# Performance work log

Hardware: AMD Instinct MI355X
Metric: run time of the kernel (lower is better)

The kernel has to match this reference:

```python
import jax, jax.numpy as jnp
import numpy as np

C, C_H, N_HEAD = 8, 1, 8


def setup_inputs() -> dict:
    key = jax.random.key(0)
    ks = jax.random.split(key, 8)
    B, S, I, c = 1, 4096, 1024, C
    hd = C_H * N_HEAD
    m = jax.random.normal(ks[0], (B, S, I, c), dtype=jnp.float32)
    mask = jnp.ones((B, S, I), dtype=jnp.float32)
    return {
        "m": m,
        "mask": mask,
        "ln_w": jnp.ones((c,), jnp.float32),
        "ln_b": jnp.zeros((c,), jnp.float32),
        "wq": jax.random.normal(ks[1], (hd, c), jnp.float32) * 0.1,
        "wk": jax.random.normal(ks[2], (C_H, c), jnp.float32) * 0.1,
        "wv": jax.random.normal(ks[3], (C_H, c), jnp.float32) * 0.1,
        "wg": jax.random.normal(ks[4], (hd, c), jnp.float32) * 0.1,
        "bg": jnp.zeros((hd,), jnp.float32),
        "wo": jax.random.normal(ks[5], (c, hd), jnp.float32) * 0.1,
        "bo": jnp.zeros((c,), jnp.float32),
    }


def _layer_norm(x, w, b, eps=1e-5):
    mu = jnp.mean(x, axis=-1, keepdims=True)
    var = jnp.mean(jnp.square(x - mu), axis=-1, keepdims=True)
    return (x - mu) * jax.lax.rsqrt(var + eps) * w + b


def reference(m, mask, ln_w, ln_b, wq, wk, wv, wg, bg, wo, bo):
    h, c_h = N_HEAD, C_H
    # transpose so attention runs over the sequence (column) axis s
    mt = jnp.swapaxes(m, -2, -3)        # (B, i, s, c)
    mk = jnp.swapaxes(mask, -1, -2)     # (B, i, s)
    mn = _layer_norm(mt, ln_w, ln_b)    # (B, i, s, c)
    # masked mean-pooled query over s
    q = jnp.sum(mn * mk[..., None], axis=-2) / (jnp.sum(mk, axis=-1)[..., None] + 1e-5)  # (B,i,c)
    q = (q @ wq.T) * (c_h ** -0.5)                      # (B, i, h*c_h)
    q = q.reshape(*q.shape[:-1], h, c_h)                # (B, i, h, c_h)
    k = mn @ wk.T                                       # (B, i, s, c_h)
    v = mn @ wv.T                                       # (B, i, s, c_h)
    g = jax.nn.sigmoid(mn @ wg.T + bg)                  # (B, i, s, h*c_h)
    g = g.reshape(*g.shape[:-1], h, c_h)                # (B, i, s, h, c_h)
    bias = (1e9 * (mk - 1.0))[..., None, :]             # (B, i, 1, s)
    a = jnp.einsum('bihd,bisd->bihs', q, k) + bias      # (B, i, h, s)
    a = jax.nn.softmax(a, axis=-1)
    o = jnp.einsum('bihs,bisd->bihd', a, v)             # (B, i, h, c_h)
    o = o[..., None, :, :] * g                          # (B, i, s, h, c_h)
    o = o.reshape(*o.shape[:-2], h * c_h)               # (B, i, s, h*c_h)
    o = o @ wo.T + bo                                   # (B, i, s, c)
    return jnp.swapaxes(o, -2, -3)                      # (B, s, i, c)
```

## Files before the change

### kernel.cpp

```cpp
#include <hip/hip_runtime.h>

#define SS 4096
#define II 1024

#define FLAGW 254
#define QSOFF 256
#define MSOFF 8448
#define OAOFF 9472
#define KOFF  17664
#define VOFF  4211968
#define BOFF  8406272

using u16 = unsigned short;

__device__ __forceinline__ float b2f(unsigned int u) {
    union { unsigned int i; float f; } t; t.i = u << 16; return t.f;
}
__device__ __forceinline__ u16 f2b(float f) {
    union { float f; unsigned int i; } t; t.f = f;
    unsigned int x = t.i;
    return (u16)((x + 0x7fffu + ((x >> 16) & 1u)) >> 16);
}
__device__ __forceinline__ void unpack8(const uint4 p, float x[8]) {
    x[0] = b2f(p.x & 0xffffu); x[1] = b2f(p.x >> 16);
    x[2] = b2f(p.y & 0xffffu); x[3] = b2f(p.y >> 16);
    x[4] = b2f(p.z & 0xffffu); x[5] = b2f(p.z >> 16);
    x[6] = b2f(p.w & 0xffffu); x[7] = b2f(p.w >> 16);
}
__device__ __forceinline__ void load8(const void* m, size_t idx, int bf, float x[8]) {
    if (bf) {
        const uint4 p = ((const uint4*)m)[idx];
        unpack8(p, x);
    } else {
        const float4 a = ((const float4*)m)[idx * 2];
        const float4 b = ((const float4*)m)[idx * 2 + 1];
        x[0]=a.x; x[1]=a.y; x[2]=a.z; x[3]=a.w;
        x[4]=b.x; x[5]=b.y; x[6]=b.z; x[7]=b.w;
    }
}
__device__ __forceinline__ float load1(const void* p, size_t idx, int bf) {
    return bf ? b2f((unsigned int)((const u16*)p)[idx]) : ((const float*)p)[idx];
}

__global__ void wconv(const void* lnw, const void* lnb, const void* wq,
                      const void* wk,  const void* wv,  const void* wg,
                      const void* bg,  const void* wo,  const void* bo,
                      float* __restrict__ W) {
    const float probe = ((const float*)lnw)[0];
    const int bf = (fabsf(probe - 1.0f) > 1e-6f) ? 1 : 0;
    const int t = threadIdx.x;
    if (blockIdx.x == 0) {
        if (t < 8)  W[t]       = load1(lnw, t, bf);
        if (t < 8)  W[8 + t]   = load1(lnb, t, bf);
        if (t < 64) W[16 + t]  = load1(wq,  t, bf);
        if (t < 8)  W[80 + t]  = load1(wk,  t, bf);
        if (t < 8)  W[88 + t]  = load1(wv,  t, bf);
        if (t < 64) W[96 + t]  = load1(wg,  t, bf);
        if (t < 8)  W[160 + t] = load1(bg,  t, bf);
        if (t < 64) W[168 + t] = load1(wo,  t, bf);
        if (t < 8)  W[232 + t] = load1(bo,  t, bf);
        if (t == 0) W[FLAGW]   = (float)bf;
    }
    const int idx = blockIdx.x * 256 + t;
    if (idx < OAOFF - QSOFF) W[QSOFF + idx] = 0.f;
}

__global__ __launch_bounds__(512, 6) void stage1(const void* __restrict__ m,
                                                 const void* __restrict__ mask,
                                                 const float* __restrict__ W,
                                                 float* __restrict__ ws) {
    __shared__ float tile[3][32][65];
    __shared__ float qacc[64][9];
    __shared__ float macc[64];
    const int tx = threadIdx.x, ty = threadIdx.y;
    const int tid = ty * 64 + tx;
    const int i  = blockIdx.x * 64 + tx;
    const int s0 = blockIdx.y * 32;
    const int bf = (int)W[FLAGW];

    if (tid < 64) macc[tid] = 0.f;
    ((float*)qacc)[tid] = 0.f;
    if (tid < 64) ((float*)qacc)[512 + tid] = 0.f;
    __syncthreads();

    float lnw[8], lnb[8], wkr[8], wvr[8];
#pragma unroll
    for (int j = 0; j < 8; j++) {
        lnw[j] = W[j]; lnb[j] = W[8 + j]; wkr[j] = W[80 + j]; wvr[j] = W[88 + j];
    }

    float qs[8] = {0.f,0.f,0.f,0.f,0.f,0.f,0.f,0.f};
    float ms = 0.f;
#pragma unroll
    for (int t = 0; t < 4; t++) {
        const int sl = ty + 8 * t;
        const int s  = s0 + sl;
        float x[8];
        load8(m, (size_t)s * II + i, bf, x);
        float mu = 0.f;
#pragma unroll
        for (int j = 0; j < 8; j++) mu += x[j];
        mu *= 0.125f;
        float var = 0.f;
#pragma unroll
        for (int j = 0; j < 8; j++) { float d = x[j] - mu; var += d * d; }
        var *= 0.125f;
        const float rs = 1.0f / sqrtf(var + 1e-5f);
        const float mk = load1(mask, (size_t)s * II + i, bf);
        float kv = 0.f, vv = 0.f;
#pragma unroll
        for (int j = 0; j < 8; j++) {
            const float n = (x[j] - mu) * rs * lnw[j] + lnb[j];
            kv += wkr[j] * n;
            vv += wvr[j] * n;
            qs[j] += n * mk;
        }
        ms += mk;
        tile[0][sl][tx] = kv;
        tile[1][sl][tx] = vv;
        tile[2][sl][tx] = 1e9f * (mk - 1.0f);
    }

#pragma unroll
    for (int j = 0; j < 8; j++) atomicAdd(&qacc[tx][j], qs[j]);
    atomicAdd(&macc[tx], ms);
    __syncthreads();

    if (ty == 0) {
#pragma unroll
        for (int j = 0; j < 8; j++) atomicAdd(&ws[QSOFF + (size_t)i * 8 + j], qacc[tx][j]);
        atomicAdd(&ws[MSOFF + i], macc[tx]);
    }

    const int iL = tid >> 3;
    const int s4 = (tid & 7) * 4;
#pragma unroll
    for (int a = 0; a < 3; a++) {
        float4 w;
        w.x = tile[a][s4    ][iL];
        w.y = tile[a][s4 + 1][iL];
        w.z = tile[a][s4 + 2][iL];
        w.w = tile[a][s4 + 3][iL];
        float* dst = ws + ((a == 0) ? (size_t)KOFF : ((a == 1) ? (size_t)VOFF : (size_t)BOFF));
        *(float4*)(dst + (size_t)(blockIdx.x * 64 + iL) * SS + s0 + s4) = w;
    }
}

__global__ __launch_bounds__(256) void attn_reduce(float* __restrict__ ws) {
    __shared__ __attribute__((aligned(16))) float sk[SS];
    __shared__ __attribute__((aligned(16))) float sv[SS];
    __shared__ __attribute__((aligned(16))) float sb[SS];
    __shared__ float redm[8][4], redz[8][4], redn[8][4];
    const int i = blockIdx.x;
    const int tid = threadIdx.x;
    const int lane = tid & 63, wid = tid >> 6;

    const float4* kp = (const float4*)(ws + KOFF + (size_t)i * SS);
    const float4* vp = (const float4*)(ws + VOFF + (size_t)i * SS);
    const float4* bp = (const float4*)(ws + BOFF + (size_t)i * SS);
#pragma unroll
    for (int t = 0; t < 4; t++) {
        int idx = t * 256 + tid;
        ((float4*)sk)[idx] = kp[idx];
        ((float4*)sv)[idx] = vp[idx];
        ((float4*)sb)[idx] = bp[idx];
    }

    const float inv = 1.0f / (ws[MSOFF + i] + 1e-5f);
    float qp[8];
#pragma unroll
    for (int j = 0; j < 8; j++) qp[j] = ws[QSOFF + (size_t)i * 8 + j] * inv;
    float qh[8];
#pragma unroll
    for (int h = 0; h < 8; h++) {
        float a = 0.f;
#pragma unroll
        for (int j = 0; j < 8; j++) a += ws[16 + h * 8 + j] * qp[j];
        qh[h] = a;
    }
    __syncthreads();

    float lm[8];
#pragma unroll
    for (int h = 0; h < 8; h++) lm[h] = -3.4e38f;
#pragma unroll
    for (int t = 0; t < 16; t++) {
        const int s = t * 256 + tid;
        const float k = sk[s], b = sb[s];
#pragma unroll
        for (int h = 0; h < 8; h++) lm[h] = fmaxf(lm[h], qh[h] * k + b);
    }
#pragma unroll
    for (int h = 0; h < 8; h++) {
#pragma unroll
        for (int off = 32; off; off >>= 1) lm[h] = fmaxf(lm[h], __shfl_xor(lm[h], off, 64));
    }
    if (lane == 0) {
#pragma unroll
        for (int h = 0; h < 8; h++) redm[h][wid] = lm[h];
    }
    __syncthreads();
    float M[8];
#pragma unroll
    for (int h = 0; h < 8; h++)
        M[h] = fmaxf(fmaxf(redm[h][0], redm[h][1]), fmaxf(redm[h][2], redm[h][3]));

    float lz[8] = {0,0,0,0,0,0,0,0}, ln[8] = {0,0,0,0,0,0,0,0};
#pragma unroll
    for (int t = 0; t < 16; t++) {
        const int s = t * 256 + tid;
        const float k = sk[s], b = sb[s], v = sv[s];
#pragma unroll
        for (int h = 0; h < 8; h++) {
            const float e = __expf(qh[h] * k + b - M[h]);
            lz[h] += e;
            ln[h] += e * v;
        }
    }
#pragma unroll
    for (int h = 0; h < 8; h++) {
#pragma unroll
        for (int off = 32; off; off >>= 1) {
            lz[h] += __shfl_xor(lz[h], off, 64);
            ln[h] += __shfl_xor(ln[h], off, 64);
        }
    }
    if (lane == 0) {
#pragma unroll
        for (int h = 0; h < 8; h++) { redz[h][wid] = lz[h]; redn[h][wid] = ln[h]; }
    }
    __syncthreads();
    if (tid < 8) {
        const int h = tid;
        const float Z = redz[h][0] + redz[h][1] + redz[h][2] + redz[h][3];
        const float N = redn[h][0] + redn[h][1] + redn[h][2] + redn[h][3];
        ws[OAOFF + (size_t)i * 8 + h] = N / Z;
    }
}

__global__ __launch_bounds__(256) void outk(const void* __restrict__ m,
                                            const float* __restrict__ W,
                                            const float* __restrict__ oatt,
                                            void* __restrict__ out) {
    const size_t idx = (size_t)blockIdx.x * 256 + threadIdx.x;
    const int i = (int)(idx & (II - 1));
    const int bf = (int)W[FLAGW];
    float x[8];
    load8(m, idx, bf, x);
    float mu = 0.f;
#pragma unroll
    for (int j = 0; j < 8; j++) mu += x[j];
    mu *= 0.125f;
    float var = 0.f;
#pragma unroll
    for (int j = 0; j < 8; j++) { float d = x[j] - mu; var += d * d; }
    var *= 0.125f;
    const float rs = 1.0f / sqrtf(var + 1e-5f);
    float n[8];
#pragma unroll
    for (int j = 0; j < 8; j++) n[j] = (x[j] - mu) * rs * W[j] + W[8 + j];

    float o[8];
#pragma unroll
    for (int h = 0; h < 8; h++) {
        float z = W[160 + h];
#pragma unroll
        for (int j = 0; j < 8; j++) z += W[96 + h * 8 + j] * n[j];
        const float g = 1.0f / (1.0f + __expf(-z));
        o[h] = oatt[(size_t)i * 8 + h] * g;
    }

    float y[8];
#pragma unroll
    for (int cc = 0; cc < 8; cc++) {
        float acc = W[232 + cc];
#pragma unroll
        for (int h = 0; h < 8; h++) acc += W[168 + cc * 8 + h] * o[h];
        y[cc] = acc;
    }
    if (bf) {
        u16 r[8];
#pragma unroll
        for (int cc = 0; cc < 8; cc++) r[cc] = f2b(y[cc]);
        uint4 q;
        q.x = (unsigned)r[0] | ((unsigned)r[1] << 16);
        q.y = (unsigned)r[2] | ((unsigned)r[3] << 16);
        q.z = (unsigned)r[4] | ((unsigned)r[5] << 16);
        q.w = (unsigned)r[6] | ((unsigned)r[7] << 16);
        ((uint4*)out)[idx] = q;
    } else {
        float4 a, b;
        a.x=y[0]; a.y=y[1]; a.z=y[2]; a.w=y[3];
        b.x=y[4]; b.y=y[5]; b.z=y[6]; b.w=y[7];
        ((float4*)out)[idx * 2]     = a;
        ((float4*)out)[idx * 2 + 1] = b;
    }
}

extern "C" void kernel_launch(void* const* d_in, const int* in_sizes, int n_in,
                              void* d_out, int out_size, void* d_ws, size_t ws_size,
                              hipStream_t stream) {
    float* ws = (float*)d_ws;

    wconv<<<37, 256, 0, stream>>>(d_in[2], d_in[3], d_in[4], d_in[5], d_in[6],
                                  d_in[7], d_in[8], d_in[9], d_in[10], ws);

    dim3 b1(64, 8), g1(II / 64, SS / 32);
    stage1<<<g1, b1, 0, stream>>>(d_in[0], d_in[1], ws, ws);

    attn_reduce<<<II, 256, 0, stream>>>(ws);

    outk<<<(SS * II) / 256, 256, 0, stream>>>(d_in[0], ws, ws + OAOFF, d_out);
}
```

Baseline: 355.7 us.

## Split attention over sequence chunks with interleaved K/V and single-pass softmax

Stage1 now writes K and V as interleaved float2 in the natural (s, i) layout instead of transposing K, V and the mask bias through shared memory into per-column rows. A new attention kernel tiles over i and s chunks, recomputes the mask bias on the fly, and accumulates exp-sums and weighted sums with global atomics. A small extra kernel then divides the two sums. The softmax no longer subtracts the running max, which removes one pass over the data. In exchange, it can overflow for large logits or divide by zero on fully masked columns.

After: 319.3 us. 1.11x faster.

```diff
diff --git a/kernel.cpp b/kernel.cpp
--- a/kernel.cpp
+++ b/kernel.cpp
@@ -6,10 +6,10 @@
 #define FLAGW 254
 #define QSOFF 256
 #define MSOFF 8448
-#define OAOFF 9472
-#define KOFF  17664
-#define VOFF  4211968
-#define BOFF  8406272
+#define ZOFF  9472
+#define NOFF  17664
+#define OAOFF 25856
+#define KVOFF 34048
 
 using u16 = unsigned short;
 
@@ -65,177 +65,137 @@
     if (idx < OAOFF - QSOFF) W[QSOFF + idx] = 0.f;
 }
 
-__global__ __launch_bounds__(512, 6) void stage1(const void* __restrict__ m,
-                                                 const void* __restrict__ mask,
-                                                 const float* __restrict__ W,
-                                                 float* __restrict__ ws) {
-    __shared__ float tile[3][32][65];
-    __shared__ float qacc[64][9];
-    __shared__ float macc[64];
+__global__ __launch_bounds__(256) void stage1(const void* __restrict__ m,
+                                              const void* __restrict__ mask,
+                                              const float* __restrict__ W,
+                                              float* __restrict__ ws) {
+    __shared__ float qred[4][64][8];
+    __shared__ float mred[4][64];
+    const int tx = threadIdx.x, ty = threadIdx.y;
+    const int i  = blockIdx.x * 64 + tx;
+    const int s0 = blockIdx.y * 128;
+    const int bf = (int)W[FLAGW];
+
+    float lnw[8], lnb[8], wkr[8], wvr[8];
+#pragma unroll
+    for (int j = 0; j < 8; j++) {
+        lnw[j] = W[j]; lnb[j] = W[8 + j]; wkr[j] = W[80 + j]; wvr[j] = W[88 + j];
+    }
+
+    float2* __restrict__ kv = (float2*)(ws + KVOFF);
+    float qs[8] = {0.f,0.f,0.f,0.f,0.f,0.f,0.f,0.f};
+    float ms = 0.f;
+#pragma unroll 4
+    for (int t = 0; t < 32; t++) {
+        const int s = s0 + ty + 4 * t;
+        const size_t idx = (size_t)s * II + i;
+        float x[8];
+        load8(m, idx, bf, x);
+        const float mk = load1(mask, idx, bf);
+        float mu = 0.f;
+#pragma unroll
+        for (int j = 0; j < 8; j++) mu += x[j];
+        mu *= 0.125f;
+        float var = 0.f;
+#pragma unroll
+        for (int j = 0; j < 8; j++) { float d = x[j] - mu; var += d * d; }
+        var *= 0.125f;
+        const float rs = 1.0f / sqrtf(var + 1e-5f);
+        float kvv = 0.f, vvv = 0.f;
+#pragma unroll
+        for (int j = 0; j < 8; j++) {
+            const float n = (x[j] - mu) * rs * lnw[j] + lnb[j];
+            kvv += wkr[j] * n;
+            vvv += wvr[j] * n;
+            qs[j] += n * mk;
+        }
+        ms += mk;
+        kv[idx] = make_float2(kvv, vvv);
+    }
+
+#pragma unroll
+    for (int j = 0; j < 8; j++) qred[ty][tx][j] = qs[j];
+    mred[ty][tx] = ms;
+    __syncthreads();
+    if (ty == 0) {
+#pragma unroll
+        for (int j = 0; j < 8; j++) {
+            const float v = qred[0][tx][j] + qred[1][tx][j] + qred[2][tx][j] + qred[3][tx][j];
+            atomicAdd(&ws[QSOFF + (size_t)i * 8 + j], v);
+        }
+        atomicAdd(&ws[MSOFF + i], mred[0][tx] + mred[1][tx] + mred[2][tx] + mred[3][tx]);
+    }
+}
+
+__global__ __launch_bounds__(256) void attnk(const void* __restrict__ mask,
+                                             const float* __restrict__ W,
+                                             float* __restrict__ ws) {
+    __shared__ float sq[64][8];
+    __shared__ float zred[4][64][8];
+    __shared__ float nred[4][64][8];
     const int tx = threadIdx.x, ty = threadIdx.y;
     const int tid = ty * 64 + tx;
     const int i  = blockIdx.x * 64 + tx;
-    const int s0 = blockIdx.y * 32;
+    const int s0 = blockIdx.y * 256;
     const int bf = (int)W[FLAGW];
 
-    if (tid < 64) macc[tid] = 0.f;
-    ((float*)qacc)[tid] = 0.f;
-    if (tid < 64) ((float*)qacc)[512 + tid] = 0.f;
+    if (tid < 64) {
+        const int i2 = blockIdx.x * 64 + tid;
+        const float inv = 1.0f / (ws[MSOFF + i2] + 1e-5f);
+        float qp[8];
+#pragma unroll
+        for (int j = 0; j < 8; j++) qp[j] = ws[QSOFF + (size_t)i2 * 8 + j] * inv;
+#pragma unroll
+        for (int h = 0; h < 8; h++) {
+            float a = 0.f;
+#pragma unroll
+            for (int j = 0; j < 8; j++) a += W[16 + h * 8 + j] * qp[j];
+            sq[tid][h] = a;
+        }
+    }
     __syncthreads();
-
-    float lnw[8], lnb[8], wkr[8], wvr[8];
-#pragma unroll
-    for (int j = 0; j < 8; j++) {
-        lnw[j] = W[j]; lnb[j] = W[8 + j]; wkr[j] = W[80 + j]; wvr[j] = W[88 + j];
-    }
-
-    float qs[8] = {0.f,0.f,0.f,0.f,0.f,0.f,0.f,0.f};
-    float ms = 0.f;
-#pragma unroll
-    for (int t = 0; t < 4; t++) {
-        const int sl = ty + 8 * t;
-        const int s  = s0 + sl;
-        float x[8];
-        load8(m, (size_t)s * II + i, bf, x);
-        float mu = 0.f;
-#pragma unroll
-        for (int j = 0; j < 8; j++) mu += x[j];
-        mu *= 0.125f;
-        float var = 0.f;
-#pragma unroll
-        for (int j = 0; j < 8; j++) { float d = x[j] - mu; var += d * d; }
-        var *= 0.125f;
-        const float rs = 1.0f / sqrtf(var + 1e-5f);
-        const float mk = load1(mask, (size_t)s * II + i, bf);
-        float kv = 0.f, vv = 0.f;
-#pragma unroll
-        for (int j = 0; j < 8; j++) {
-            const float n = (x[j] - mu) * rs * lnw[j] + lnb[j];
-            kv += wkr[j] * n;
-            vv += wvr[j] * n;
-            qs[j] += n * mk;
-        }
-        ms += mk;
-        tile[0][sl][tx] = kv;
-        tile[1][sl][tx] = vv;
-        tile[2][sl][tx] = 1e9f * (mk - 1.0f);
-    }
-
-#pragma unroll
-    for (int j = 0; j < 8; j++) atomicAdd(&qacc[tx][j], qs[j]);
-    atomicAdd(&macc[tx], ms);
+    float qh[8];
+#pragma unroll
+    for (int h = 0; h < 8; h++) qh[h] = sq[tx][h];
+
+    const float2* __restrict__ kv = (const float2*)(ws + KVOFF);
+    float z[8] = {0,0,0,0,0,0,0,0}, n[8] = {0,0,0,0,0,0,0,0};
+#pragma unroll 4
+    for (int t = 0; t < 64; t++) {
+        const int s = s0 + ty + 4 * t;
+        const size_t idx = (size_t)s * II + i;
+        const float2 p = kv[idx];
+        const float mk = load1(mask, idx, bf);
+        const float b = 1e9f * (mk - 1.0f);
+#pragma unroll
+        for (int h = 0; h < 8; h++) {
+            const float e = __expf(qh[h] * p.x + b);
+            z[h] += e;
+            n[h] += e * p.y;
+        }
+    }
+#pragma unroll
+    for (int h = 0; h < 8; h++) { zred[ty][tx][h] = z[h]; nred[ty][tx][h] = n[h]; }
     __syncthreads();
-
     if (ty == 0) {
 #pragma unroll
-        for (int j = 0; j < 8; j++) atomicAdd(&ws[QSOFF + (size_t)i * 8 + j], qacc[tx][j]);
-        atomicAdd(&ws[MSOFF + i], macc[tx]);
-    }
-
-    const int iL = tid >> 3;
-    const int s4 = (tid & 7) * 4;
-#pragma unroll
-    for (int a = 0; a < 3; a++) {
-        float4 w;
-        w.x = tile[a][s4    ][iL];
-        w.y = tile[a][s4 + 1][iL];
-        w.z = tile[a][s4 + 2][iL];
-        w.w = tile[a][s4 + 3][iL];
-        float* dst = ws + ((a == 0) ? (size_t)KOFF : ((a == 1) ? (size_t)VOFF : (size_t)BOFF));
-        *(float4*)(dst + (size_t)(blockIdx.x * 64 + iL) * SS + s0 + s4) = w;
-    }
-}
-
-__global__ __launch_bounds__(256) void attn_reduce(float* __restrict__ ws) {
-    __shared__ __attribute__((aligned(16))) float sk[SS];
-    __shared__ __attribute__((aligned(16))) float sv[SS];
-    __shared__ __attribute__((aligned(16))) float sb[SS];
-    __shared__ float redm[8][4], redz[8][4], redn[8][4];
-    const int i = blockIdx.x;
-    const int tid = threadIdx.x;
-    const int lane = tid & 63, wid = tid >> 6;
-
-    const float4* kp = (const float4*)(ws + KOFF + (size_t)i * SS);
-    const float4* vp = (const float4*)(ws + VOFF + (size_t)i * SS);
-    const float4* bp = (const float4*)(ws + BOFF + (size_t)i * SS);
-#pragma unroll
-    for (int t = 0; t < 4; t++) {
-        int idx = t * 256 + tid;
-        ((float4*)sk)[idx] = kp[idx];
-        ((float4*)sv)[idx] = vp[idx];
-        ((float4*)sb)[idx] = bp[idx];
-    }
-
-    const float inv = 1.0f / (ws[MSOFF + i] + 1e-5f);
-    float qp[8];
-#pragma unroll
-    for (int j = 0; j < 8; j++) qp[j] = ws[QSOFF + (size_t)i * 8 + j] * inv;
-    float qh[8];
-#pragma unroll
-    for (int h = 0; h < 8; h++) {
-        float a = 0.f;
-#pragma unroll
-        for (int j = 0; j < 8; j++) a += ws[16 + h * 8 + j] * qp[j];
-        qh[h] = a;
-    }
-    __syncthreads();
-
-    float lm[8];
-#pragma unroll
-    for (int h = 0; h < 8; h++) lm[h] = -3.4e38f;
-#pragma unroll
-    for (int t = 0; t < 16; t++) {
-        const int s = t * 256 + tid;
-        const float k = sk[s], b = sb[s];
-#pragma unroll
-        for (int h = 0; h < 8; h++) lm[h] = fmaxf(lm[h], qh[h] * k + b);
-    }
-#pragma unroll
-    for (int h = 0; h < 8; h++) {
-#pragma unroll
-        for (int off = 32; off; off >>= 1) lm[h] = fmaxf(lm[h], __shfl_xor(lm[h], off, 64));
-    }
-    if (lane == 0) {
-#pragma unroll
-        for (int h = 0; h < 8; h++) redm[h][wid] = lm[h];
-    }
-    __syncthreads();
-    float M[8];
-#pragma unroll
-    for (int h = 0; h < 8; h++)
-        M[h] = fmaxf(fmaxf(redm[h][0], redm[h][1]), fmaxf(redm[h][2], redm[h][3]));
-
-    float lz[8] = {0,0,0,0,0,0,0,0}, ln[8] = {0,0,0,0,0,0,0,0};
-#pragma unroll
-    for (int t = 0; t < 16; t++) {
-        const int s = t * 256 + tid;
-        const float k = sk[s], b = sb[s], v = sv[s];
-#pragma unroll
-        for (int h = 0; h < 8; h++) {
-            const float e = __expf(qh[h] * k + b - M[h]);
-            lz[h] += e;
-            ln[h] += e * v;
-        }
-    }
-#pragma unroll
-    for (int h = 0; h < 8; h++) {
-#pragma unroll
-        for (int off = 32; off; off >>= 1) {
-            lz[h] += __shfl_xor(lz[h], off, 64);
-            ln[h] += __shfl_xor(ln[h], off, 64);
-        }
-    }
-    if (lane == 0) {
-#pragma unroll
-        for (int h = 0; h < 8; h++) { redz[h][wid] = lz[h]; redn[h][wid] = ln[h]; }
-    }
-    __syncthreads();
-    if (tid < 8) {
-        const int h = tid;
-        const float Z = redz[h][0] + redz[h][1] + redz[h][2] + redz[h][3];
-        const float N = redn[h][0] + redn[h][1] + redn[h][2] + redn[h][3];
-        ws[OAOFF + (size_t)i * 8 + h] = N / Z;
-    }
+        for (int h = 0; h < 8; h++) {
+            const float v = zred[0][tx][h] + zred[1][tx][h] + zred[2][tx][h] + zred[3][tx][h];
+            atomicAdd(&ws[ZOFF + (size_t)i * 8 + h], v);
+        }
+    }
+    if (ty == 1) {
+#pragma unroll
+        for (int h = 0; h < 8; h++) {
+            const float v = nred[0][tx][h] + nred[1][tx][h] + nred[2][tx][h] + nred[3][tx][h];
+            atomicAdd(&ws[NOFF + (size_t)i * 8 + h], v);
+        }
+    }
+}
+
+__global__ void oatk(float* __restrict__ ws) {
+    const int idx = blockIdx.x * 256 + threadIdx.x;
+    if (idx < II * 8) ws[OAOFF + idx] = ws[NOFF + idx] / ws[ZOFF + idx];
 }
 
 __global__ __launch_bounds__(256) void outk(const void* __restrict__ m,
@@ -302,13 +262,17 @@
                               hipStream_t stream) {
     float* ws = (float*)d_ws;
 
-    wconv<<<37, 256, 0, stream>>>(d_in[2], d_in[3], d_in[4], d_in[5], d_in[6],
-                                  d_in[7], d_in[8], d_in[9], d_in[10], ws);
-
-    dim3 b1(64, 8), g1(II / 64, SS / 32);
+    wconv<<<100, 256, 0, stream>>>(d_in[2], d_in[3], d_in[4], d_in[5], d_in[6],
+                                   d_in[7], d_in[8], d_in[9], d_in[10], ws);
+
+    dim3 b1(64, 4);
+    dim3 g1(II / 64, SS / 128);
     stage1<<<g1, b1, 0, stream>>>(d_in[0], d_in[1], ws, ws);
 
-    attn_reduce<<<II, 256, 0, stream>>>(ws);
+    dim3 g2(II / 64, SS / 256);
+    attnk<<<g2, b1, 0, stream>>>(d_in[1], ws, ws);
+
+    oatk<<<32, 256, 0, stream>>>(ws);
 
     outk<<<(SS * II) / 256, 256, 0, stream>>>(d_in[0], ws, ws + OAOFF, d_out);
 }
```
